# Kernel tuning notes

Measured on AMD Instinct MI355X. Metric: run time of the kernel, lower is better.

Reference implementation:

```python
import jax, jax.numpy as jnp
import numpy as np

C = 0.1            # args.hyp_c
EPS_PROJ = 4e-3    # hyptorch project eps for float32
MIN_NORM = 1e-5
NUM_HEADS = 12


def _norm(x):
    return jnp.maximum(jnp.linalg.norm(x, axis=-1, keepdims=True), MIN_NORM)


def expmap0(u, c):
    sqrt_c = c ** 0.5
    u_norm = _norm(u)
    return jnp.tanh(sqrt_c * u_norm) * u / (sqrt_c * u_norm)


def project(x, c):
    sqrt_c = c ** 0.5
    norm = _norm(x)
    maxnorm = (1.0 - EPS_PROJ) / sqrt_c
    return jnp.where(norm > maxnorm, x / norm * maxnorm, x)


def logmap0(y, c):
    sqrt_c = c ** 0.5
    y_norm = _norm(y)
    arg = jnp.clip(sqrt_c * y_norm, -1 + 1e-5, 1 - 1e-5)
    artanh = 0.5 * jnp.log((1 + arg) / (1 - arg))
    return y / (y_norm * sqrt_c) * artanh


def qkv_attention(x, wq, bq, wk, bk, wv, bv, num_heads):
    # x: [B, N, D]; weights in torch Linear convention [out, in]
    B, N, D = x.shape
    dh = D // num_heads
    q = (x @ wq.T + bq).reshape(B, N, num_heads, dh)
    k = (x @ wk.T + bk).reshape(B, N, num_heads, dh)
    v = (x @ wv.T + bv).reshape(B, N, num_heads, dh)
    # NOTE: original has no 1/sqrt(dh) scaling — keep faithful
    att = jnp.einsum('bnhd,bmhd->bhnm', q, k)
    att = jax.nn.softmax(att, axis=-1)
    out = jnp.einsum('bhnm,bmhd->bnhd', att, v)
    return out.reshape(B, N, D)


def setup_inputs() -> dict:
    key = jax.random.key(0)
    ks = jax.random.split(key, 7)
    B, N, D = 8, 1024, 768
    s = 0.02
    return {
        'x':   jax.random.normal(ks[0], (B, N, D), jnp.float32),
        'w_q': jax.random.normal(ks[1], (3, D, D), jnp.float32) * s,
        'b_q': jax.random.normal(ks[2], (3, D), jnp.float32) * s,
        'w_k': jax.random.normal(ks[3], (3, D, D), jnp.float32) * s,
        'b_k': jax.random.normal(ks[4], (3, D), jnp.float32) * s,
        'w_v': jax.random.normal(ks[5], (3, D, D), jnp.float32) * s,
        'b_v': jax.random.normal(ks[6], (3, D), jnp.float32) * s,
    }


def reference(x, w_q, b_q, w_k, b_k, w_v, b_v):
    # branch 0: euclidean; branch 1: hyperbolic (ToPoincare); branch 2: spherical (FromPoincare)
    x_e = x
    x_h = project(expmap0(x, C), C)
    x_s = logmap0(x, C)
    out = 0.0
    for i, xb in enumerate((x_e, x_h, x_s)):
        out = out + qkv_attention(xb, w_q[i], b_q[i], w_k[i], b_k[i],
                                  w_v[i], b_v[i], NUM_HEADS)
    return out
```

## Files before the change

### kernel.cpp

```cpp
#include <hip/hip_runtime.h>
#include <hip/hip_bf16.h>
#include <cstdint>
#include <cstddef>

#define B_   8
#define N_   1024
#define D_   768
#define H_   12
#define DH_  64
#define M_   (B_ * N_)
#define WSZ_ (D_ * D_)

typedef __bf16 bf16;
typedef bf16  bf16x8  __attribute__((ext_vector_type(8)));
typedef bf16  bf16x4  __attribute__((ext_vector_type(4)));
typedef float floatx4 __attribute__((ext_vector_type(4)));

#define MFMA16 __builtin_amdgcn_mfma_f32_16x16x32_bf16

__device__ __forceinline__ float exp2_fast(float x) {
    float r;
    asm("v_exp_f32 %0, %1" : "=v"(r) : "v"(x));
    return r;
}

__device__ __forceinline__ void gload_lds16(const void* g, void* l) {
    __builtin_amdgcn_global_load_lds(
        (const __attribute__((address_space(1))) unsigned int*)g,
        (__attribute__((address_space(3))) unsigned int*)l, 16, 0, 0);
}

__global__ __launch_bounds__(256) void prep_x(const float* __restrict__ x,
                                              bf16* __restrict__ xbf,
                                              float* __restrict__ sc ) {
    int row = blockIdx.x;
    int tid = threadIdx.x;
    const float* xr = x + (size_t)row * D_;
    bf16* xo = xbf + (size_t)row * D_;
    float v0 = xr[tid], v1 = xr[tid + 256], v2 = xr[tid + 512];
    xo[tid]       = (bf16)v0;
    xo[tid + 256] = (bf16)v1;
    xo[tid + 512] = (bf16)v2;
    float ss = v0 * v0 + v1 * v1 + v2 * v2;
    for (int off = 32; off; off >>= 1) ss += __shfl_xor(ss, off, 64);
    __shared__ float red[4];
    if ((tid & 63) == 0) red[tid >> 6] = ss;
    __syncthreads();
    if (tid == 0) {
        float t2 = red[0] + red[1] + red[2] + red[3];
        float t  = sqrtf(t2);
        const float scst = 0.31622776601683794f;
        float un = fmaxf(t, 1e-5f);
        float s1 = tanhf(scst * un) / (scst * un);
        float nh = fmaxf(t * s1, 1e-5f);
        float maxnorm = (1.0f - 4e-3f) / scst;
        float sh = (nh > maxnorm) ? s1 * (maxnorm / nh) : s1;
        float arg = fminf(scst * un, 1.0f - 1e-5f);
        float artanh = 0.5f * logf((1.0f + arg) / (1.0f - arg));
        float ssc = artanh / (un * scst);
        sc[row]      = sh;
        sc[M_ + row] = ssc;
    }
}

__global__ __launch_bounds__(256) void prep_w(const float* __restrict__ wq,
                                              const float* __restrict__ wk,
                                              const float* __restrict__ wv,
                                              bf16* __restrict__ wbf) {
    size_t i = ((size_t)blockIdx.x * 256 + threadIdx.x) * 4;
    int z = (int)(i / WSZ_);
    int r = (int)(i % WSZ_);
    int branch = z / 3, t = z % 3;
    const float* src = (t == 0 ? wq : t == 1 ? wk : wv) + (size_t)branch * WSZ_ + r;
    float4 f = *(const float4*)src;
    bf16x4 o = { (bf16)f.x, (bf16)f.y, (bf16)f.z, (bf16)f.w };
    *(bf16x4*)(wbf + i) = o;
}

#define NT9 12

#define STG(buf, mat, half, t) do {                                          \
    const bf16* _src = (mat) ? wbf : xbf;                                    \
    int _rb = ((mat) ? bn0 : bm0) + (half) * 128 + w * 16 + (lane >> 2);     \
    const bf16* _g = _src + (size_t)_rb * D_ + (t) * 64 + (lane & 3) * 8;    \
    bf16* _l = &L[buf][mat][half][0][w * 16][0];                             \
    gload_lds16(_g, _l);                                                     \
    gload_lds16(_g + 32, _l + 4096);                                         \
} while (0)

#define LOADA(buf, mh) do {                                                  \
    _Pragma("unroll") for (int fi = 0; fi < 4; fi++)                         \
    _Pragma("unroll") for (int kk = 0; kk < 2; kk++)                         \
        afr[fi][kk] = *(const bf16x8*)(&L[buf][0][wm][kk][(mh)*64 + fi*16 + c15][quad*8]); \
} while (0)

#define LOADB(buf, nh) do {                                                  \
    _Pragma("unroll") for (int fj = 0; fj < 2; fj++)                         \
    _Pragma("unroll") for (int kk = 0; kk < 2; kk++)                         \
        bfr[nh][fj][kk] = *(const bf16x8*)(&L[buf][1][wn>>1][kk][(wn&1)*64 + (nh)*32 + fj*16 + c15][quad*8]); \
} while (0)

#define MFMACL(mh, nh) do {                                                  \
    __builtin_amdgcn_s_setprio(1);                                           \
    _Pragma("unroll") for (int fi = 0; fi < 4; fi++)                         \
    _Pragma("unroll") for (int fj = 0; fj < 2; fj++)                         \
    _Pragma("unroll") for (int kk = 0; kk < 2; kk++)                         \
        acc[(mh)*4 + fi][(nh)*2 + fj] =                                      \
            MFMA16(afr[fi][kk], bfr[nh][fj][kk], acc[(mh)*4 + fi][(nh)*2 + fj], 0, 0, 0); \
    __builtin_amdgcn_s_setprio(0);                                           \
} while (0)

#define BAR() __builtin_amdgcn_s_barrier()
#define VMW4() asm volatile("s_waitcnt vmcnt(4)" ::: "memory")

__global__ __launch_bounds__(512, 2) void gemm_qkv9(
        const bf16* __restrict__ xbf, const bf16* __restrict__ wbf,
        const float* __restrict__ bq, const float* __restrict__ bk,
        const float* __restrict__ bv, const float* __restrict__ sc,
        bf16* __restrict__ qkv) {
    int bid = blockIdx.x;
    int v = (bid & 7) * 108 + (bid >> 3);
    int bx = v >> 5;
    int by = v & 31;
    int bn0 = bx * 256;
    int bm0 = by * 256;

    __shared__ bf16 L[2][2][2][2][128][32];

    int tid = threadIdx.x;
    int w = tid >> 6, lane = tid & 63;
    int wm = w >> 2, wn = w & 3;
    int quad = lane >> 4, c15 = lane & 15;

    bf16x8 afr[4][2];
    bf16x8 bfr[2][2][2];
    floatx4 acc[8][4];
#pragma unroll
    for (int i = 0; i < 8; i++)
#pragma unroll
        for (int j = 0; j < 4; j++) acc[i][j] = (floatx4){0.f, 0.f, 0.f, 0.f};

    STG(0, 0, 0, 0); STG(0, 0, 1, 0); STG(0, 1, 0, 0); STG(0, 1, 1, 0);
    STG(1, 1, 0, 1); STG(1, 1, 1, 1);
    VMW4();
    BAR();

    for (int it = 0; it < 6; it++) {
        int t1 = 2 * it + 1;
        bool st2 = (it < 5);
        LOADA(0, 0); LOADB(0, 0);
        STG(1, 0, 0, t1);
        BAR(); MFMACL(0, 0); BAR();
        LOADB(0, 1);
        STG(1, 0, 1, t1);
        BAR(); MFMACL(0, 1); BAR();
        LOADA(0, 1);
        if (st2) STG(0, 1, 0, t1 + 1);
        BAR(); MFMACL(1, 1); BAR();
        if (st2) STG(0, 1, 1, t1 + 1);
        VMW4();
        BAR(); MFMACL(1, 0); BAR();
        LOADA(1, 0); LOADB(1, 0);
        if (st2) STG(0, 0, 0, t1 + 1);
        BAR(); MFMACL(0, 0); BAR();
        LOADB(1, 1);
        if (st2) STG(0, 0, 1, t1 + 1);
        BAR(); MFMACL(0, 1); BAR();
        LOADA(1, 1);
        if (st2) STG(1, 1, 0, t1 + 2);
        BAR(); MFMACL(1, 1); BAR();
        if (st2) STG(1, 1, 1, t1 + 2);
        VMW4();
        BAR(); MFMACL(1, 0); BAR();
    }

    int gz = bn0 / 768;
    int branch = gz / 3, t = gz % 3;
    int colz0 = (bn0 % 768) + wn * 64;
    const float* bias = (t == 0 ? bq : t == 1 ? bk : bv) + branch * D_;
    const float* scb = (branch == 0) ? nullptr : sc + (size_t)(branch - 1) * M_;
    float bj[4];
#pragma unroll
    for (int fj = 0; fj < 4; fj++) bj[fj] = bias[colz0 + fj * 16 + c15];
    bf16* outz = qkv + (size_t)gz * M_ * D_;
#pragma unroll
    for (int fi = 0; fi < 8; fi++) {
        int rowbase = bm0 + wm * 128 + fi * 16 + quad * 4;
        float4 sv = scb ? *(const float4*)(scb + rowbase)
                        : (float4){1.f, 1.f, 1.f, 1.f};
        float svr[4] = { sv.x, sv.y, sv.z, sv.w };
        if (t == 2) {
            int b = rowbase >> 10, nn = rowbase & 1023;
#pragma unroll
            for (int fj = 0; fj < 4; fj++) {
                int col = colz0 + fj * 16 + c15;
                int h = col >> 6, dd = col & 63;
                bf16x4 pkv;
#pragma unroll
                for (int r = 0; r < 4; r++)
                    pkv[r] = (bf16)(svr[r] * acc[fi][fj][r] + bj[fj]);
                *(bf16x4*)(outz + (((size_t)(b * H_ + h) * 64 + dd) << 10) + nn) = pkv;
            }
        } else {
#pragma unroll
            for (int r = 0; r < 4; r++) {
                bf16* orow = outz + (size_t)(rowbase + r) * D_;
#pragma unroll
                for (int fj = 0; fj < 4; fj++)
                    orow[colz0 + fj * 16 + c15] = (bf16)(svr[r] * acc[fi][fj][r] + bj[fj]);
            }
        }
    }
}

#define BM 128
#define BN 128
#define BK 32
__global__ __launch_bounds__(256) void gemm_qkv(
        const bf16* __restrict__ xbf, const bf16* __restrict__ wbf_all,
        const float* __restrict__ bq, const float* __restrict__ bk,
        const float* __restrict__ bv, const float* __restrict__ sc,
        int zoff, bf16* __restrict__ qkv) {
    int gz = zoff + blockIdx.z;
    int branch = gz / 3, t = gz % 3;
    const bf16*  wsrc = wbf_all + (size_t)gz * WSZ_;
    const float* bias = (t == 0 ? bq : t == 1 ? bk : bv) + branch * D_;
    bf16* out = qkv + (size_t)blockIdx.z * M_ * D_;
    int bm0 = blockIdx.y * BM;
    int bn0 = blockIdx.x * BN;

    __shared__ bf16 lA[BM * BK];
    __shared__ bf16 lB[BN * BK];

    int tid = threadIdx.x;
    int w = tid >> 6, lane = tid & 63;
    int wr = w >> 1, wc = w & 1;
    int quad = lane >> 4, c15 = lane & 15;
    int lrow = lane >> 2;
    int lcol = (lane & 3) * 8;

    floatx4 acc[4][4];
    for (int i = 0; i < 4; i++)
        for (int j = 0; j < 4; j++)
            acc[i][j] = (floatx4){0.f, 0.f, 0.f, 0.f};

    for (int k0 = 0; k0 < D_; k0 += BK) {
        const bf16* ga = xbf  + ((size_t)(bm0 + w * 32 + lrow) * D_ + k0 + lcol);
        const bf16* gb = wsrc + ((size_t)(bn0 + w * 32 + lrow) * D_ + k0 + lcol);
        gload_lds16(ga,           (char*)lA + w * 2048);
        gload_lds16(ga + 16 * D_, (char*)lA + w * 2048 + 1024);
        gload_lds16(gb,           (char*)lB + w * 2048);
        gload_lds16(gb + 16 * D_, (char*)lB + w * 2048 + 1024);
        __syncthreads();

        int arow = wr * 64 + c15;
        int brow = wc * 64 + c15;
        int kq = quad * 8;
        bf16x8 af[4], bfm[4];
        for (int i = 0; i < 4; i++) af[i]  = *(const bf16x8*)(lA + (arow + i * 16) * BK + kq);
        for (int j = 0; j < 4; j++) bfm[j] = *(const bf16x8*)(lB + (brow + j * 16) * BK + kq);
        for (int i = 0; i < 4; i++)
            for (int j = 0; j < 4; j++)
                acc[i][j] = MFMA16(af[i], bfm[j], acc[i][j], 0, 0, 0);
        __syncthreads();
    }

    const float* scb = (branch == 0) ? nullptr : sc + (size_t)(branch - 1) * M_;
    float bj[4];
    for (int j = 0; j < 4; j++) bj[j] = bias[bn0 + wc * 64 + j * 16 + c15];
    for (int i = 0; i < 4; i++) {
        int gRow0 = bm0 + wr * 64 + i * 16 + quad * 4;
        float s[4];
        for (int r = 0; r < 4; r++) s[r] = scb ? scb[gRow0 + r] : 1.0f;
        if (t == 2) {
            int b = gRow0 >> 10, nn = gRow0 & 1023;
            for (int j = 0; j < 4; j++) {
                int col = bn0 + wc * 64 + j * 16 + c15;
                int h = col >> 6, dd = col & 63;
                bf16x4 pkv;
                for (int r = 0; r < 4; r++)
                    pkv[r] = (bf16)(s[r] * acc[i][j][r] + bj[j]);
                *(bf16x4*)(out + (((size_t)(b * H_ + h) * 64 + dd) << 10) + nn) = pkv;
            }
        } else {
            for (int r = 0; r < 4; r++) {
                bf16* orow = out + (size_t)(gRow0 + r) * D_;
                for (int j = 0; j < 4; j++) {
                    int gCol = bn0 + wc * 64 + j * 16 + c15;
                    orow[gCol] = (bf16)(s[r] * acc[i][j][r] + bj[j]);
                }
            }
        }
    }
}

#define LDK 72
__global__ __launch_bounds__(256) void attn(const bf16* __restrict__ qkv,
                                            float* __restrict__ out) {
    int qt = blockIdx.x;
    int bh = blockIdx.y;
    int br = blockIdx.z;
    int batch = bh / H_, head = bh % H_;
    int n0 = qt * 128;
    int tid = threadIdx.x, w = tid >> 6, lane = tid & 63;
    int quad = lane >> 4, c15 = lane & 15;

    const bf16* base = qkv + (size_t)br * 3 * M_ * D_;
    size_t baseRow = (size_t)batch * N_;
    int colOff = head * DH_;
    const bf16* qb = base;
    const bf16* kb = base + (size_t)M_ * D_;
    const bf16* vR = base + (size_t)2 * M_ * D_
                   + ((size_t)(batch * H_ + head) * 64 + c15) * 1024 + quad * 8;

    __shared__ bf16 sK[64 * LDK];
    __shared__ bf16 sP[4][32 * LDK];
    bf16* sPw = sP[w];

    bf16x8 aq[2][2];
#pragma unroll
    for (int h = 0; h < 2; h++) {
        const bf16* qp = qb + ((baseRow + n0 + w * 32 + h * 16 + c15) * D_ + colOff + quad * 8);
        aq[h][0] = *(const bf16x8*)qp;
        aq[h][1] = *(const bf16x8*)(qp + 32);
#pragma unroll
        for (int f = 0; f < 2; f++)
#pragma unroll
            for (int i = 0; i < 8; i++)
                aq[h][f][i] = (bf16)((float)aq[h][f][i] * 1.4426950408889634f);
    }

    float m_sw[2] = { 0.f, 0.f };
    float l_sw[2] = { 0.f, 0.f };
    floatx4 o_acc[2][4];
#pragma unroll
    for (int h = 0; h < 2; h++)
#pragma unroll
        for (int j = 0; j < 4; j++) o_acc[h][j] = (floatx4){0.f, 0.f, 0.f, 0.f};

    int kkey = tid >> 3;
    int kcol = (tid & 7) << 3;
    const bf16* kg = kb + (baseRow + kkey) * D_ + colOff + kcol;
    bf16x8 kr0 = *(const bf16x8*)kg;
    bf16x8 kr1 = *(const bf16x8*)(kg + (size_t)32 * D_);

    for (int kt = 0; kt < 16; kt++) {
        int m0 = kt * 64;
        if (kt) __syncthreads();
        *(bf16x8*)(sK + kkey * LDK + kcol)        = kr0;
        *(bf16x8*)(sK + (kkey + 32) * LDK + kcol) = kr1;
        __syncthreads();
        if (kt < 15) {
            const bf16* kgn = kg + (size_t)(kt + 1) * 64 * D_;
            kr0 = *(const bf16x8*)kgn;
            kr1 = *(const bf16x8*)(kgn + (size_t)32 * D_);
        }
        bf16x8 vf0[4], vf1[4];
#pragma unroll
        for (int j = 0; j < 4; j++) {
            const bf16* vp = vR + (size_t)(j * 16) * 1024 + m0;
            vf0[j] = *(const bf16x8*)vp;
            vf1[j] = *(const bf16x8*)(vp + 32);
        }

        floatx4 sfr[2][4];
        __builtin_amdgcn_s_setprio(1);
#pragma unroll
        for (int j = 0; j < 4; j++) {
            const bf16* kp = sK + (j * 16 + c15) * LDK + quad * 8;
            bf16x8 k0 = *(const bf16x8*)kp;
            bf16x8 k1 = *(const bf16x8*)(kp + 32);
#pragma unroll
            for (int h = 0; h < 2; h++) {
                floatx4 z = (floatx4){0.f, 0.f, 0.f, 0.f};
                z = MFMA16(k0, aq[h][0], z, 0, 0, 0);
                z = MFMA16(k1, aq[h][1], z, 0, 0, 0);
                sfr[h][j] = z;
            }
        }
        __builtin_amdgcn_s_setprio(0);

#pragma unroll
        for (int h = 0; h < 2; h++) {
            float mx = sfr[h][0][0];
#pragma unroll
            for (int j = 0; j < 4; j++)
#pragma unroll
                for (int r = 0; r < 4; r++) mx = fmaxf(mx, sfr[h][j][r]);
            if (__any(mx > m_sw[h] + 11.0f)) {
                float mr = fmaxf(mx, __shfl_xor(mx, 16, 64));
                mr = fmaxf(mr, __shfl_xor(mr, 32, 64));
                float mnew = fmaxf(m_sw[h], mr);
                float alpha = exp2_fast(m_sw[h] - mnew);
                l_sw[h] *= alpha;
                m_sw[h] = mnew;
#pragma unroll
                for (int r = 0; r < 4; r++) {
                    float a = __shfl(alpha, quad * 4 + r, 64);
#pragma unroll
                    for (int j = 0; j < 4; j++) o_acc[h][j][r] *= a;
                }
            }
            float m = m_sw[h];
            float sum = 0.f;
            bf16x4 pk[4];
#pragma unroll
            for (int j = 0; j < 4; j++)
#pragma unroll
                for (int r = 0; r < 4; r++) {
                    float p = exp2_fast(sfr[h][j][r] - m);
                    sum += p;
                    pk[j][r] = (bf16)p;
                }
            sum += __shfl_xor(sum, 16, 64);
            sum += __shfl_xor(sum, 32, 64);
            l_sw[h] += sum;
            bf16* pw = sPw + (h * 16 + c15) * LDK;
#pragma unroll
            for (int j = 0; j < 4; j++)
                *(bf16x4*)(pw + j * 16 + quad * 4) = pk[j];
        }

        asm volatile("s_waitcnt lgkmcnt(0)" ::: "memory");
        __builtin_amdgcn_sched_barrier(0);

        bf16x8 ap[2][2];
#pragma unroll
        for (int h = 0; h < 2; h++) {
            const bf16* pp = sPw + (h * 16 + c15) * LDK + quad * 8;
            ap[h][0] = *(const bf16x8*)pp;
            ap[h][1] = *(const bf16x8*)(pp + 32);
        }
        __builtin_amdgcn_s_setprio(1);
#pragma unroll
        for (int j = 0; j < 4; j++) {
#pragma unroll
            for (int h = 0; h < 2; h++) {
                o_acc[h][j] = MFMA16(ap[h][0], vf0[j], o_acc[h][j], 0, 0, 0);
                o_acc[h][j] = MFMA16(ap[h][1], vf1[j], o_acc[h][j], 0, 0, 0);
            }
        }
        __builtin_amdgcn_s_setprio(0);
    }

#pragma unroll
    for (int h = 0; h < 2; h++) {
        float inv = 1.0f / l_sw[h];
#pragma unroll
        for (int r = 0; r < 4; r++) {
            float iv = __shfl(inv, quad * 4 + r, 64);
            int row = n0 + w * 32 + h * 16 + quad * 4 + r;
            float* op = out + ((size_t)batch * N_ + row) * D_ + colOff;
#pragma unroll
            for (int j = 0; j < 4; j++) {
                float v = o_acc[h][j][r] * iv;
                int col = j * 16 + c15;
                unsafeAtomicAdd(op + col, v);
            }
        }
    }
}

extern "C" void kernel_launch(void* const* d_in, const int* in_sizes, int n_in,
                              void* d_out, int out_size, void* d_ws, size_t ws_size,
                              hipStream_t stream) {
    const float* x  = (const float*)d_in[0];
    const float* wq = (const float*)d_in[1];
    const float* bq = (const float*)d_in[2];
    const float* wk = (const float*)d_in[3];
    const float* bk = (const float*)d_in[4];
    const float* wv = (const float*)d_in[5];
    const float* bv = (const float*)d_in[6];
    float* out = (float*)d_out;

    char* ws = (char*)d_ws;
    bf16*  xbf = (bf16*)ws;
    bf16*  wbf = (bf16*)(ws + 12582912);
    float* sc  = (float*)(ws + 12582912 + 10616832);
    bf16*  qkv = (bf16*)(ws + 12582912 + 10616832 + 65536);

    const size_t matB = (size_t)M_ * D_ * 2;
    const size_t need_all = 12582912 + 10616832 + 65536 + 9 * matB;

    hipMemsetAsync(d_out, 0, out_size, stream);
    hipLaunchKernelGGL(prep_x, dim3(M_), dim3(256), 0, stream, x, xbf, sc);
    hipLaunchKernelGGL(prep_w, dim3((9 * WSZ_ / 4) / 256), dim3(256), 0, stream, wq, wk, wv, wbf);

    if (ws_size >= need_all) {
        hipLaunchKernelGGL(gemm_qkv9, dim3(864), dim3(512), 0, stream,
                           xbf, wbf, bq, bk, bv, sc, qkv);
        hipLaunchKernelGGL(attn, dim3(N_ / 128, B_ * H_, 3), dim3(256), 0, stream,
                           qkv, out);
    } else {
        for (int br = 0; br < 3; br++) {
            hipLaunchKernelGGL(gemm_qkv, dim3(D_ / BN, M_ / BM, 3), dim3(256), 0, stream,
                               xbf, wbf, bq, bk, bv, sc, br * 3, qkv);
            hipLaunchKernelGGL(attn, dim3(N_ / 128, B_ * H_, 1), dim3(256), 0, stream,
                               qkv, out);
        }
    }
}
```

Baseline: 414.0 us.

## Double-buffer K and V tiles in LDS via direct global-to-LDS loads with XOR swizzle

The attention kernel now stages both K and V tiles in double-buffered shared memory, filled by direct global-to-LDS loads that fetch the next tile while the current one is being computed. Previously K went through registers into a single padded buffer, and V fragments were loaded per thread straight from global memory every iteration. An XOR swizzle on the row offset replaces padding to avoid bank conflicts. The max and sum reductions are also rewritten as balanced trees to shorten dependency chains. The changes add shared-memory footprint and rely on correct vmcnt and barrier ordering between the two buffers.

```diff
diff --git a/kernel.cpp b/kernel.cpp
--- a/kernel.cpp
+++ b/kernel.cpp
@@ -294,7 +294,7 @@
     }
 }
 
-#define LDK 72
+#define LDKP 72
 __global__ __launch_bounds__(256) void attn(const bf16* __restrict__ qkv,
                                             float* __restrict__ out) {
     int qt = blockIdx.x;
@@ -308,14 +308,23 @@
     const bf16* base = qkv + (size_t)br * 3 * M_ * D_;
     size_t baseRow = (size_t)batch * N_;
     int colOff = head * DH_;
-    const bf16* qb = base;
-    const bf16* kb = base + (size_t)M_ * D_;
-    const bf16* vR = base + (size_t)2 * M_ * D_
-                   + ((size_t)(batch * H_ + head) * 64 + c15) * 1024 + quad * 8;
-
-    __shared__ bf16 sK[64 * LDK];
-    __shared__ bf16 sP[4][32 * LDK];
+    const bf16* qb  = base;
+    const bf16* kb  = base + (size_t)M_ * D_;
+    const bf16* vtb = base + (size_t)2 * M_ * D_
+                    + ((size_t)(batch * H_ + head) * 64) * 1024;
+
+    __shared__ bf16 sK[2][64][64];
+    __shared__ bf16 sV[2][64][64];
+    __shared__ bf16 sP[4][32 * LDKP];
     bf16* sPw = sP[w];
+
+    int lr  = lane >> 3;
+    int swz = ((lane & 7) ^ lr) * 8;
+    const bf16* kgl = kb  + (baseRow + w * 8 + lr) * D_ + colOff + swz;
+    const bf16* vgl = vtb + ((size_t)(w * 8 + lr)) * 1024 + swz;
+
+    int s0 = (quad ^ (c15 & 7)) * 8;
+    int s1 = s0 ^ 32;
 
     bf16x8 aq[2][2];
 #pragma unroll
@@ -338,38 +347,30 @@
 #pragma unroll
         for (int j = 0; j < 4; j++) o_acc[h][j] = (floatx4){0.f, 0.f, 0.f, 0.f};
 
-    int kkey = tid >> 3;
-    int kcol = (tid & 7) << 3;
-    const bf16* kg = kb + (baseRow + kkey) * D_ + colOff + kcol;
-    bf16x8 kr0 = *(const bf16x8*)kg;
-    bf16x8 kr1 = *(const bf16x8*)(kg + (size_t)32 * D_);
-
+    gload_lds16(kgl,                      &sK[0][w * 8][0]);
+    gload_lds16(kgl + (size_t)32 * D_,    &sK[0][32 + w * 8][0]);
+    gload_lds16(vgl,                      &sV[0][w * 8][0]);
+    gload_lds16(vgl + 32 * 1024,          &sV[0][32 + w * 8][0]);
+    asm volatile("s_waitcnt vmcnt(0)" ::: "memory");
+    __builtin_amdgcn_s_barrier();
+
+    int buf = 0;
     for (int kt = 0; kt < 16; kt++) {
-        int m0 = kt * 64;
-        if (kt) __syncthreads();
-        *(bf16x8*)(sK + kkey * LDK + kcol)        = kr0;
-        *(bf16x8*)(sK + (kkey + 32) * LDK + kcol) = kr1;
-        __syncthreads();
         if (kt < 15) {
-            const bf16* kgn = kg + (size_t)(kt + 1) * 64 * D_;
-            kr0 = *(const bf16x8*)kgn;
-            kr1 = *(const bf16x8*)(kgn + (size_t)32 * D_);
-        }
-        bf16x8 vf0[4], vf1[4];
-#pragma unroll
-        for (int j = 0; j < 4; j++) {
-            const bf16* vp = vR + (size_t)(j * 16) * 1024 + m0;
-            vf0[j] = *(const bf16x8*)vp;
-            vf1[j] = *(const bf16x8*)(vp + 32);
+            int m1 = (kt + 1) * 64;
+            gload_lds16(kgl + (size_t)m1 * D_,        &sK[buf ^ 1][w * 8][0]);
+            gload_lds16(kgl + (size_t)(m1 + 32) * D_, &sK[buf ^ 1][32 + w * 8][0]);
+            gload_lds16(vgl + m1,                     &sV[buf ^ 1][w * 8][0]);
+            gload_lds16(vgl + 32 * 1024 + m1,         &sV[buf ^ 1][32 + w * 8][0]);
         }
 
         floatx4 sfr[2][4];
         __builtin_amdgcn_s_setprio(1);
 #pragma unroll
         for (int j = 0; j < 4; j++) {
-            const bf16* kp = sK + (j * 16 + c15) * LDK + quad * 8;
-            bf16x8 k0 = *(const bf16x8*)kp;
-            bf16x8 k1 = *(const bf16x8*)(kp + 32);
+            const bf16* kp = &sK[buf][j * 16 + c15][0];
+            bf16x8 k0 = *(const bf16x8*)(kp + s0);
+            bf16x8 k1 = *(const bf16x8*)(kp + s1);
 #pragma unroll
             for (int h = 0; h < 2; h++) {
                 floatx4 z = (floatx4){0.f, 0.f, 0.f, 0.f};
@@ -382,11 +383,11 @@
 
 #pragma unroll
         for (int h = 0; h < 2; h++) {
-            float mx = sfr[h][0][0];
-#pragma unroll
-            for (int j = 0; j < 4; j++)
-#pragma unroll
-                for (int r = 0; r < 4; r++) mx = fmaxf(mx, sfr[h][j][r]);
+            float q0 = fmaxf(fmaxf(sfr[h][0][0], sfr[h][0][1]), fmaxf(sfr[h][0][2], sfr[h][0][3]));
+            float q1 = fmaxf(fmaxf(sfr[h][1][0], sfr[h][1][1]), fmaxf(sfr[h][1][2], sfr[h][1][3]));
+            float q2 = fmaxf(fmaxf(sfr[h][2][0], sfr[h][2][1]), fmaxf(sfr[h][2][2], sfr[h][2][3]));
+            float q3 = fmaxf(fmaxf(sfr[h][3][0], sfr[h][3][1]), fmaxf(sfr[h][3][2], sfr[h][3][3]));
+            float mx = fmaxf(fmaxf(q0, q1), fmaxf(q2, q3));
             if (__any(mx > m_sw[h] + 11.0f)) {
                 float mr = fmaxf(mx, __shfl_xor(mx, 16, 64));
                 mr = fmaxf(mr, __shfl_xor(mr, 32, 64));
@@ -402,20 +403,25 @@
                 }
             }
             float m = m_sw[h];
-            float sum = 0.f;
+            float pe[4][4];
             bf16x4 pk[4];
 #pragma unroll
             for (int j = 0; j < 4; j++)
 #pragma unroll
                 for (int r = 0; r < 4; r++) {
                     float p = exp2_fast(sfr[h][j][r] - m);
-                    sum += p;
+                    pe[j][r] = p;
                     pk[j][r] = (bf16)p;
                 }
+            float f0 = (pe[0][0] + pe[0][1]) + (pe[0][2] + pe[0][3]);
+            float f1 = (pe[1][0] + pe[1][1]) + (pe[1][2] + pe[1][3]);
+            float f2 = (pe[2][0] + pe[2][1]) + (pe[2][2] + pe[2][3]);
+            float f3 = (pe[3][0] + pe[3][1]) + (pe[3][2] + pe[3][3]);
+            float sum = (f0 + f1) + (f2 + f3);
             sum += __shfl_xor(sum, 16, 64);
             sum += __shfl_xor(sum, 32, 64);
             l_sw[h] += sum;
-            bf16* pw = sPw + (h * 16 + c15) * LDK;
+            bf16* pw = sPw + (h * 16 + c15) * LDKP;
 #pragma unroll
             for (int j = 0; j < 4; j++)
                 *(bf16x4*)(pw + j * 16 + quad * 4) = pk[j];
@@ -427,20 +433,29 @@
         bf16x8 ap[2][2];
 #pragma unroll
         for (int h = 0; h < 2; h++) {
-            const bf16* pp = sPw + (h * 16 + c15) * LDK + quad * 8;
+            const bf16* pp = sPw + (h * 16 + c15) * LDKP + quad * 8;
             ap[h][0] = *(const bf16x8*)pp;
             ap[h][1] = *(const bf16x8*)(pp + 32);
         }
         __builtin_amdgcn_s_setprio(1);
 #pragma unroll
         for (int j = 0; j < 4; j++) {
+            const bf16* vp = &sV[buf][j * 16 + c15][0];
+            bf16x8 v0 = *(const bf16x8*)(vp + s0);
+            bf16x8 v1 = *(const bf16x8*)(vp + s1);
 #pragma unroll
             for (int h = 0; h < 2; h++) {
-                o_acc[h][j] = MFMA16(ap[h][0], vf0[j], o_acc[h][j], 0, 0, 0);
-                o_acc[h][j] = MFMA16(ap[h][1], vf1[j], o_acc[h][j], 0, 0, 0);
+                o_acc[h][j] = MFMA16(ap[h][0], v0, o_acc[h][j], 0, 0, 0);
+                o_acc[h][j] = MFMA16(ap[h][1], v1, o_acc[h][j], 0, 0, 0);
             }
         }
         __builtin_amdgcn_s_setprio(0);
+
+        if (kt < 15) {
+            asm volatile("s_waitcnt vmcnt(0)" ::: "memory");
+            __builtin_amdgcn_s_barrier();
+            buf ^= 1;
+        }
     }
 
 #pragma unroll
```

Result: faster. 362.8 us (-12.4%).
